# Optimization experiments

Hardware: AMD Instinct MI355X
Metric: run time of the kernel (lower is better)

Reference implementation:

```python
import jax, jax.numpy as jnp
import numpy as np

B, N, DIM = 8, 512, 768
H, DH = 12, 64
INNER = H * DH
MLP = 3072
DEPTH = 4
EPS = 1e-5
LS = 0.1  # LayerScale init_eps for depth <= 18


def _ln(x, scale):
    # flax LayerNorm(use_bias=False): (x-mean)/sqrt(var+eps) * scale
    mu = jnp.mean(x, axis=-1, keepdims=True)
    var = jnp.mean(jnp.square(x - mu), axis=-1, keepdims=True)
    return (x - mu) * jax.lax.rsqrt(var + EPS) * scale


def setup_inputs() -> dict:
    key = jax.random.key(0)
    ks = jax.random.split(key, 13)
    s = 0.02
    inp = {
        "x": jax.random.normal(ks[0], (B, N, DIM), jnp.float32),
        "ln1": jnp.ones((DEPTH, DIM), jnp.float32),
        "Wq": jax.random.normal(ks[1], (DEPTH, DIM, INNER), jnp.float32) * s,
        "Wkv": jax.random.normal(ks[2], (DEPTH, DIM, 2 * INNER), jnp.float32) * s,
        "mix_pre": jax.random.normal(ks[3], (DEPTH, H, H), jnp.float32) * 0.1,
        "mix_post": jax.random.normal(ks[4], (DEPTH, H, H), jnp.float32) * 0.1,
        "Wo": jax.random.normal(ks[5], (DEPTH, INNER, DIM), jnp.float32) * s,
        "bo": jnp.zeros((DEPTH, DIM), jnp.float32),
        "ln2": jnp.ones((DEPTH, DIM), jnp.float32),
        "W1": jax.random.normal(ks[6], (DEPTH, DIM, MLP), jnp.float32) * s,
        "b1": jnp.zeros((DEPTH, MLP), jnp.float32),
        "W2": jax.random.normal(ks[7], (DEPTH, MLP, DIM), jnp.float32) * s,
        "b2": jnp.zeros((DEPTH, DIM), jnp.float32),
    }
    return inp


def _block(x, p):
    ln1, Wq, Wkv, mp, mq, Wo, bo, ln2, W1, b1, W2, b2 = p
    scale = DH ** -0.5
    h = _ln(x, ln1)
    q = h @ Wq                                  # [b,n,inner]
    kv = h @ Wkv
    k, v = jnp.split(kv, 2, axis=-1)
    def to_heads(t):
        return t.reshape(B, N, H, DH).transpose(0, 2, 1, 3)  # b h n d
    q, k, v = to_heads(q), to_heads(k), to_heads(v)
    dots = jnp.einsum('bhid,bhjd->bhij', q, k) * scale
    dots = jnp.einsum('bhij,hg->bgij', dots, mp)   # talking-heads pre-softmax
    attn = jax.nn.softmax(dots, axis=-1)
    attn = jnp.einsum('bhij,hg->bgij', attn, mq)   # talking-heads post-softmax
    o = jnp.einsum('bhij,bhjd->bhid', attn, v)
    o = o.transpose(0, 2, 1, 3).reshape(B, N, INNER)
    x = (o @ Wo + bo) * LS + x
    h2 = _ln(x, ln2)
    x = ((jax.nn.gelu(h2 @ W1 + b1) @ W2) + b2) * LS + x
    return x, None


def reference(x, ln1, Wq, Wkv, mix_pre, mix_post, Wo, bo, ln2, W1, b1, W2, b2):
    params = (ln1, Wq, Wkv, mix_pre, mix_post, Wo, bo, ln2, W1, b1, W2, b2)
    out, _ = jax.lax.scan(_block, x, params)
    return out
```

## Files before the change

### kernel.cpp

```cpp
#include <hip/hip_runtime.h>


#define LSCALE 0.1f

typedef __bf16 bf16;
typedef __bf16 bf16x8 __attribute__((ext_vector_type(8)));
typedef __bf16 bf16x4 __attribute__((ext_vector_type(4)));
typedef unsigned short ushort4v __attribute__((ext_vector_type(4)));
typedef float  f32x4  __attribute__((ext_vector_type(4)));

__device__ __forceinline__ void g2l16(const void* g, void* l) {
    __builtin_amdgcn_global_load_lds(
        (const __attribute__((address_space(1))) void*)g,
        (__attribute__((address_space(3))) void*)l, 16, 0, 0);
}

__device__ __forceinline__ void tconv_tile(int T, int t,
    const float* __restrict__ Wq, const float* __restrict__ Wkv,
    const float* __restrict__ Wo, const float* __restrict__ W1,
    const float* __restrict__ W2, bf16* __restrict__ WtAll, char* pmem)
{
    float (*st)[65] = (float(*)[65])pmem;
    const int L = T / 1728;
    int bx = T - L * 1728;
    bf16* WtL = WtAll + (long)L * 7077888;
    const float* src; bf16* dst; int K, N, ntn;
    if (bx < 144) {
        src = Wq + (long)L * 589824;   dst = WtL;            K = 768;  N = 768;  ntn = 12;
    } else if (bx < 432) {
        bx -= 144;
        src = Wkv + (long)L * 1179648; dst = WtL + 589824;   K = 768;  N = 1536; ntn = 24;
    } else if (bx < 576) {
        bx -= 432;
        src = Wo + (long)L * 589824;   dst = WtL + 1769472;  K = 768;  N = 768;  ntn = 12;
    } else if (bx < 1152) {
        bx -= 576;
        src = W1 + (long)L * 2359296;  dst = WtL + 2359296;  K = 768;  N = 3072; ntn = 48;
    } else {
        bx -= 1152;
        src = W2 + (long)L * 2359296;  dst = WtL + 4718592;  K = 3072; N = 768;  ntn = 12;
    }
    const int n0 = (bx % ntn) * 64, k0 = (bx / ntn) * 64;
    const int r = t >> 4, c4 = (t & 15) * 4;
#pragma unroll
    for (int rr = 0; rr < 4; rr++) {
        const f32x4 v = *(const f32x4*)(src + (long)(k0 + r + rr * 16) * N + n0 + c4);
        st[r + rr * 16][c4 + 0] = v[0];
        st[r + rr * 16][c4 + 1] = v[1];
        st[r + rr * 16][c4 + 2] = v[2];
        st[r + rr * 16][c4 + 3] = v[3];
    }
    __syncthreads();
    const int kc = (t & 7) * 8;
#pragma unroll
    for (int p = 0; p < 2; p++) {
        const int n = p * 32 + (t >> 3);
        bf16x8 o;
#pragma unroll
        for (int e = 0; e < 8; e++) o[e] = (bf16)st[kc + e][n];
        *(bf16x8*)(dst + (long)(n0 + n) * K + k0 + kc) = o;
    }
}

template<int EPI, bool PLANA = false, bool RID = false>
__global__ __launch_bounds__(256, 2)
void gemm_bt(const bf16* __restrict__ A, int lda, long saz1, long saz2,
             const bf16* __restrict__ Bt, int ldb, long sbz1, long sbz2,
             void* __restrict__ Cv, int ldc, long scz1, long scz2,
             int M, int N, int K, int zmod,
             const float* __restrict__ bias, float scale,
             int mt, int nt, int rbase,
             const float* __restrict__ tWq, const float* __restrict__ tWkv,
             const float* __restrict__ tWo, const float* __restrict__ tW1,
             const float* __restrict__ tW2, bf16* __restrict__ tWt)
{
    __shared__ __align__(16) char smem[35840];
    bf16* As = (bf16*)smem;
    bf16* Bs = (bf16*)(smem + 16384);
    bf16* Cs = (bf16*)smem;

    int bm, bn, z;
    if constexpr (RID) {
        const int nbg = mt * nt * zmod;
        const int bx = blockIdx.x;
        if (bx >= nbg) {
            tconv_tile(rbase + bx - nbg, threadIdx.x,
                       tWq, tWkv, tWo, tW1, tW2, tWt, smem);
            return;
        }
        bm = bx % mt;
        const int r = bx / mt;
        bn = r % nt;
        z  = r / nt;
    } else {
        bm = blockIdx.x; bn = blockIdx.y; z = blockIdx.z;
    }

    const int z1 = z / zmod, z2 = z - z1 * zmod;
    const bf16* Ab = A  + saz1 * (long)z1 + saz2 * (long)z2;
    const bf16* Bb = Bt + sbz1 * (long)z1 + sbz2 * (long)z2;

    const int m0 = bm * 128, n0 = bn * 128;
    const int tid = threadIdx.x, w = tid >> 6, l = tid & 63;
    const int wr = (w >> 1) * 64, wc = (w & 1) * 64;
    const int lr = l & 15, lq = l >> 4;
    const int srow = l >> 2, scol8 = (l & 3) * 8;

    long abase = 0;
    if constexpr (PLANA)
        abase = (long)(m0 >> 9) * 393216 + (long)((m0 & 511) + w * 32) * 64;

    f32x4 acc[4][4];
#pragma unroll
    for (int i = 0; i < 4; i++)
#pragma unroll
        for (int j = 0; j < 4; j++)
#pragma unroll
            for (int r = 0; r < 4; r++) acc[i][j][r] = 0.f;

    for (int k0 = 0; k0 < K; k0 += 64) {
        const bf16* Ag;
        int ldaa;
        if constexpr (PLANA) {
            Ag = Ab + abase + ((long)(k0 >> 6)) * 32768;
            ldaa = 64;
        } else {
            Ag = Ab + (long)(m0 + w * 32) * lda + k0;
            ldaa = lda;
        }
        const bf16* Bg = Bb + (long)(n0 + w * 32) * ldb + k0;
        g2l16(Ag + (long)srow * ldaa + scol8,             As + w * 1024);
        g2l16(Ag + (long)(srow + 16) * ldaa + scol8,      As + w * 1024 + 512);
        g2l16(Ag + (long)srow * ldaa + 32 + scol8,        As + 4096 + w * 1024);
        g2l16(Ag + (long)(srow + 16) * ldaa + 32 + scol8, As + 4096 + w * 1024 + 512);
        g2l16(Bg + (long)srow * ldb + scol8,             Bs + w * 1024);
        g2l16(Bg + (long)(srow + 16) * ldb + scol8,      Bs + w * 1024 + 512);
        g2l16(Bg + (long)srow * ldb + 32 + scol8,        Bs + 4096 + w * 1024);
        g2l16(Bg + (long)(srow + 16) * ldb + 32 + scol8, Bs + 4096 + w * 1024 + 512);
        __syncthreads();

#pragma unroll
        for (int hh = 0; hh < 2; hh++) {
            bf16x8 fa[4], fb[4];
#pragma unroll
            for (int i = 0; i < 4; i++)
                fa[i] = *(const bf16x8*)(As + hh * 4096 + (wr + i * 16 + lr) * 32 + lq * 8);
#pragma unroll
            for (int i = 0; i < 4; i++)
                fb[i] = *(const bf16x8*)(Bs + hh * 4096 + (wc + i * 16 + lr) * 32 + lq * 8);
#pragma unroll
            for (int mi = 0; mi < 4; mi++)
#pragma unroll
                for (int ni = 0; ni < 4; ni++)
                    acc[mi][ni] = __builtin_amdgcn_mfma_f32_16x16x32_bf16(
                        fa[mi], fb[ni], acc[mi][ni], 0, 0, 0);
        }
        __syncthreads();
    }

#pragma unroll
    for (int ni = 0; ni < 4; ni++) {
        const int col = wc + ni * 16 + lr;
        float bv = 0.f;
        if (EPI == 1) bv = bias[n0 + col];
#pragma unroll
        for (int mi = 0; mi < 4; mi++) {
#pragma unroll
            for (int r = 0; r < 4; r++) {
                const int row = wr + mi * 16 + lq * 4 + r;
                float v = acc[mi][ni][r];
                if (EPI == 0) {
                    v *= scale;
                } else if (EPI == 1) {
                    const float xx = v + bv;
                    const float u  = 0.7978845608f * (xx + 0.044715f * xx * xx * xx);
                    const float th = 1.f - 2.f / (__expf(2.f * u) + 1.f);
                    v = 0.5f * xx * (1.f + th);
                }
                Cs[row * 136 + col] = (bf16)v;
            }
        }
    }
    __syncthreads();

    const long cb = scz1 * (long)z1 + scz2 * (long)z2;
    const int rrow = tid >> 4, cg = tid & 15;
#pragma unroll
    for (int p = 0; p < 8; p++) {
        const int row = p * 16 + rrow;
        const bf16x8 v = *(const bf16x8*)(Cs + row * 136 + cg * 8);
        *(bf16x8*)((bf16*)Cv + cb + (long)(m0 + row) * ldc + n0 + cg * 8) = v;
    }
}

template<int PLANO>
__global__ __launch_bounds__(256, 4)
void gemm_av(const bf16* __restrict__ S, const bf16* __restrict__ qkvc,
             bf16* __restrict__ oc)
{
    __shared__ __align__(16) char av_smem[9728];
    bf16* As  = (bf16*)av_smem;
    bf16* Bst = (bf16*)(av_smem + 4096);
    bf16* Cs  = (bf16*)av_smem;

    const int z = blockIdx.y, b = z / 12, g = z - b * 12;
    const bf16* Ab;
    int sld;
    if constexpr (PLANO) {
        Ab = S + (long)b * 3145728 + g * 512;
        sld = 6144;
    } else {
        Ab = S + (long)z * 262144;
        sld = 512;
    }
    const bf16* Bb = qkvc + (long)b * 1179648 + 1536 + g * 64;

    const int i0 = blockIdx.x * 64;
    const int tid = threadIdx.x, w = tid >> 6, l = tid & 63;
    const int lr = l & 15, lq = l >> 4;
    const int srow = l >> 2, scol8 = (l & 3) * 8;
    const int kp = tid >> 4, dq = tid & 15;
    const int kcol = ((((kp >> 2) ^ ((dq >> 1) & 3)) << 3) | ((kp & 3) << 1));

    f32x4 acc[4];
#pragma unroll
    for (int j = 0; j < 4; j++)
#pragma unroll
        for (int r = 0; r < 4; r++) acc[j][r] = 0.f;

    unsigned short* Bw = (unsigned short*)Bst;

    for (int k0 = 0; k0 < 512; k0 += 32) {
        const bf16* Ag = Ab + (long)(i0 + w * 16) * sld + k0;
        g2l16(Ag + (long)srow * sld + scol8, As + w * 512);

        const bf16* Bg = Bb + (long)(k0 + 2 * kp) * 2304 + dq * 4;
        ushort4v u0 = *(const ushort4v*)(Bg);
        ushort4v u1 = *(const ushort4v*)(Bg + 2304);
#pragma unroll
        for (int r = 0; r < 4; r++) {
            unsigned p = (unsigned)u0[r] | ((unsigned)u1[r] << 16);
            *(unsigned*)(Bw + (dq * 4 + r) * 40 + kcol) = p;
        }
        __syncthreads();

        bf16x8 fa = *(const bf16x8*)(As + (w * 16 + lr) * 32 + lq * 8);
        bf16x8 fb[4];
#pragma unroll
        for (int i = 0; i < 4; i++) {
            const int d = i * 16 + lr;
            fb[i] = *(const bf16x8*)(Bst + d * 40 + ((lq ^ ((d >> 3) & 3)) << 3));
        }
#pragma unroll
        for (int ni = 0; ni < 4; ni++)
            acc[ni] = __builtin_amdgcn_mfma_f32_16x16x32_bf16(
                fa, fb[ni], acc[ni], 0, 0, 0);
        __syncthreads();
    }

    if constexpr (PLANO) {
#pragma unroll
        for (int ni = 0; ni < 4; ni++)
#pragma unroll
            for (int r = 0; r < 4; r++)
                Cs[(w * 16 + lq * 4 + r) * 68 + ni * 16 + lr] = (bf16)acc[ni][r];
        __syncthreads();
        const int rr = tid >> 2, c16 = (tid & 3) * 16;
        bf16* orow = oc + ((long)z * 512 + i0 + rr) * 64 + c16;
        *(bf16x8*)(orow)     = *(const bf16x8*)(Cs + rr * 68 + c16);
        *(bf16x8*)(orow + 8) = *(const bf16x8*)(Cs + rr * 68 + c16 + 8);
    } else {
        bf16* Cb = oc + (long)b * 1179648 + g * 64;
#pragma unroll
        for (int ni = 0; ni < 4; ni++) {
            const int gc = ni * 16 + lr;
#pragma unroll
            for (int r = 0; r < 4; r++) {
                const int gr = i0 + w * 16 + lq * 4 + r;
                Cb[(long)gr * 2304 + gc] = (bf16)acc[ni][r];
            }
        }
    }
}

__global__ __launch_bounds__(256)
void tconv_k(const float* __restrict__ in, bf16* __restrict__ out,
             int K, int N)
{
    __shared__ float t[32][33];
    const int n0 = blockIdx.x * 32, k0 = blockIdx.y * 32;
    const int x = threadIdx.x, y = threadIdx.y;
#pragma unroll
    for (int yy = 0; yy < 4; yy++)
        t[y + yy * 8][x] = in[(long)(k0 + y + yy * 8) * N + n0 + x];
    __syncthreads();
#pragma unroll
    for (int yy = 0; yy < 4; yy++)
        out[(long)(n0 + y + yy * 8) * K + k0 + x] = (bf16)t[x][y + yy * 8];
}

__global__ __launch_bounds__(256)
void pre2_k(const float* __restrict__ Wq, const float* __restrict__ Wkv,
            const float* __restrict__ Wo, const float* __restrict__ W1,
            const float* __restrict__ W2, bf16* __restrict__ WtAll,
            const float* __restrict__ x, float* __restrict__ xf,
            const float* __restrict__ gam, bf16* __restrict__ hout)
{
    __shared__ __align__(16) char pmem[16640];
    const int bxg = blockIdx.x;
    const int t = threadIdx.x;
    if (bxg < 432) {
        tconv_tile(bxg, t, Wq, Wkv, Wo, W1, W2, WtAll, pmem);
    } else {
        const int row = bxg - 432;
        float* ps  = (float*)pmem;
        float* pss = (float*)pmem + 4;
        const float* xin = x + (long)row * 768;
        float* xr = xf + (long)row * 768;
        float v[3];
#pragma unroll
        for (int i = 0; i < 3; i++) {
            const int c = t + i * 256;
            const float xv = xin[c];
            xr[c] = xv;
            v[i] = xv;
        }
        float s  = v[0] + v[1] + v[2];
        float ss = v[0] * v[0] + v[1] * v[1] + v[2] * v[2];
#pragma unroll
        for (int off = 32; off; off >>= 1) {
            s  += __shfl_xor(s, off);
            ss += __shfl_xor(ss, off);
        }
        const int wv = t >> 6, l = t & 63;
        if (l == 0) { ps[wv] = s; pss[wv] = ss; }
        __syncthreads();
        s  = ps[0] + ps[1] + ps[2] + ps[3];
        ss = pss[0] + pss[1] + pss[2] + pss[3];
        const float mu = s * (1.f / 768.f);
        const float rs = rsqrtf(ss * (1.f / 768.f) - mu * mu + 1e-5f);
        bf16* orow = hout + (long)row * 768;
#pragma unroll
        for (int i = 0; i < 3; i++) {
            const int c = t + i * 256;
            orow[c] = (bf16)((v[i] - mu) * rs * gam[c]);
        }
    }
}

__global__ __launch_bounds__(256)
void lnres_k(float* __restrict__ xf, const bf16* __restrict__ P0,
             const bf16* __restrict__ P1, const float* __restrict__ bias,
             const float* __restrict__ gam, bf16* __restrict__ out,
             const float* __restrict__ src)
{
    const int row = blockIdx.x, t = threadIdx.x;
    float* xr = xf + (long)row * 768;
    float v[3];
#pragma unroll
    for (int i = 0; i < 3; i++) {
        const int c = t + i * 256;
        float xv;
        if (src) {
            xv = src[(long)row * 768 + c];
            xr[c] = xv;
        } else if (P0) {
            xv = xr[c] + LSCALE * ((float)P0[(long)row * 768 + c] +
                                   (float)P1[(long)row * 768 + c] + bias[c]);
            xr[c] = xv;
        } else {
            xv = xr[c];
        }
        v[i] = xv;
    }
    float s  = v[0] + v[1] + v[2];
    float ss = v[0] * v[0] + v[1] * v[1] + v[2] * v[2];
#pragma unroll
    for (int off = 32; off; off >>= 1) {
        s  += __shfl_xor(s, off);
        ss += __shfl_xor(ss, off);
    }
    __shared__ float ps[4], pss[4];
    const int wv = t >> 6, l = t & 63;
    if (l == 0) { ps[wv] = s; pss[wv] = ss; }
    __syncthreads();
    s  = ps[0] + ps[1] + ps[2] + ps[3];
    ss = pss[0] + pss[1] + pss[2] + pss[3];
    const float mu = s * (1.f / 768.f);
    const float rs = rsqrtf(ss * (1.f / 768.f) - mu * mu + 1e-5f);
    bf16* orow = out + (long)row * 768;
#pragma unroll
    for (int i = 0; i < 3; i++) {
        const int c = t + i * 256;
        orow[c] = (bf16)((v[i] - mu) * rs * gam[c]);
    }
}

__global__ __launch_bounds__(256)
void outres_k(const float* __restrict__ xf, const bf16* __restrict__ P0,
              const bf16* __restrict__ P1, const float* __restrict__ bias,
              float* __restrict__ out)
{
    const long i4 = ((long)blockIdx.x * 256 + threadIdx.x) * 4;
    const int c = (int)(i4 % 768);
    const f32x4 xv = *(const f32x4*)(xf + i4);
    const bf16x4 p0 = *(const bf16x4*)(P0 + i4);
    const bf16x4 p1 = *(const bf16x4*)(P1 + i4);
    const f32x4 bv = *(const f32x4*)(bias + c);
    f32x4 o;
#pragma unroll
    for (int e = 0; e < 4; e++)
        o[e] = xv[e] + LSCALE * ((float)p0[e] + (float)p1[e] + bv[e]);
    *(f32x4*)(out + i4) = o;
}

template<int CONTIG>
__global__ __launch_bounds__(256)
void mixsm_k(bf16* __restrict__ S, const float* __restrict__ mp,
             const float* __restrict__ mq)
{
    __shared__ float buf[12][512];
    __shared__ float rds[12];
    const int b = blockIdx.y, i = blockIdx.x, t = threadIdx.x;
    const long pstr = CONTIG ? 512 : 262144;
    bf16* Sb = CONTIG ? S + ((long)b * 512 + i) * 6144
                      : S + ((long)b * 12 * 512 + i) * 512;

    float s0[12], s1[12];
#pragma unroll
    for (int h = 0; h < 12; h++) {
        union { unsigned u; bf16 v[2]; } p;
        p.u = *(const unsigned*)(Sb + h * pstr + 2 * t);
        s0[h] = (float)p.v[0];
        s1[h] = (float)p.v[1];
    }
#pragma unroll
    for (int g = 0; g < 12; g++) {
        float a0 = 0.f, a1 = 0.f;
#pragma unroll
        for (int h = 0; h < 12; h++) {
            const float m = mp[h * 12 + g];
            a0 += s0[h] * m;
            a1 += s1[h] * m;
        }
        *(float2*)(&buf[g][2 * t]) = make_float2(a0, a1);
    }
    __syncthreads();

    const int wv = t >> 6, l = t & 63;
    for (int g = wv; g < 12; g += 4) {
        float mx = -3.0e38f;
#pragma unroll
        for (int k = 0; k < 8; k++) mx = fmaxf(mx, buf[g][l + 64 * k]);
#pragma unroll
        for (int off = 32; off; off >>= 1) mx = fmaxf(mx, __shfl_xor(mx, off));
        float sm = 0.f;
#pragma unroll
        for (int k = 0; k < 8; k++) {
            const float e = __expf(buf[g][l + 64 * k] - mx);
            buf[g][l + 64 * k] = e;
            sm += e;
        }
#pragma unroll
        for (int off = 32; off; off >>= 1) sm += __shfl_xor(sm, off);
        if (l == 0) rds[g] = 1.f / sm;
    }
    __syncthreads();

    float e0[12], e1[12];
#pragma unroll
    for (int h = 0; h < 12; h++) {
        const float2 ee = *(const float2*)(&buf[h][2 * t]);
        const float rd = rds[h];
        e0[h] = ee.x * rd;
        e1[h] = ee.y * rd;
    }
#pragma unroll
    for (int g = 0; g < 12; g++) {
        float a0 = 0.f, a1 = 0.f;
#pragma unroll
        for (int h = 0; h < 12; h++) {
            const float m = mq[h * 12 + g];
            a0 += e0[h] * m;
            a1 += e1[h] * m;
        }
        union { unsigned u; bf16 v[2]; } p;
        p.v[0] = (bf16)a0;
        p.v[1] = (bf16)a1;
        *(unsigned*)(Sb + g * pstr + 2 * t) = p.u;
    }
}

extern "C" void kernel_launch(void* const* d_in, const int* in_sizes, int n_in,
                              void* d_out, int out_size, void* d_ws, size_t ws_size,
                              hipStream_t stream)
{
    (void)in_sizes; (void)n_in; (void)out_size;
    const float* x   = (const float*)d_in[0];
    const float* ln1 = (const float*)d_in[1];
    const float* Wq  = (const float*)d_in[2];
    const float* Wkv = (const float*)d_in[3];
    const float* mp  = (const float*)d_in[4];
    const float* mq  = (const float*)d_in[5];
    const float* Wo  = (const float*)d_in[6];
    const float* bo  = (const float*)d_in[7];
    const float* ln2 = (const float*)d_in[8];
    const float* W1  = (const float*)d_in[9];
    const float* b1  = (const float*)d_in[10];
    const float* W2  = (const float*)d_in[11];
    const float* b2  = (const float*)d_in[12];

    char* ws = (char*)d_ws;
    float* xf  = (float*)(ws);
    bf16* h    = (bf16*)(ws + 12582912);
    bf16* qkv  = (bf16*)(ws + 18874368);
    bf16* S    = (bf16*)(ws + 37748736);
    bf16* mid  = S;
    bf16* P0   = h;
    bf16* P1w2 = qkv;
    bf16* P1wo = S;
    const long P1W2_OFF = 3145728;
    const long P1WO_OFF = 12582912;

    const dim3 tb(32, 8);

    if (ws_size >= 150994944ull) {
        bf16* WtAll = (bf16*)(ws + 88080384);
        bf16* oP    = (bf16*)(ws + 144703488);

        pre2_k<<<4528, 256, 0, stream>>>(Wq, Wkv, Wo, W1, W2, WtAll,
                                         x, xf, ln1, h);

        for (int L = 0; L < 4; L++) {
            bf16* WtL = WtAll + (long)L * 7077888;

            if (L > 0)
                lnres_k<<<4096, 256, 0, stream>>>(xf, P0, P1w2, b2 + (L - 1) * 768,
                                                  ln1 + L * 768, h, nullptr);

            if (L == 0)
                gemm_bt<0, false, true><<<576 + 1728, 256, 0, stream>>>(
                    h, 768, 0, 0, WtL, 768, 0, 0,
                    qkv, 2304, 0, 0, 4096, 2304, 768, 1, nullptr, 1.f,
                    32, 18, 432, Wq, Wkv, Wo, W1, W2, WtAll);
            else
                gemm_bt<0><<<dim3(32, 18, 1), 256, 0, stream>>>(
                    h, 768, 0, 0, WtL, 768, 0, 0,
                    qkv, 2304, 0, 0, 4096, 2304, 768, 1, nullptr, 1.f,
                    0, 0, 0, nullptr, nullptr, nullptr, nullptr, nullptr, nullptr);

            gemm_bt<0><<<dim3(4, 4, 96), 256, 0, stream>>>(
                qkv,       2304, 1179648, 64,
                qkv + 768, 2304, 1179648, 64,
                S,         6144, 3145728, 512,
                512, 512, 64, 12, nullptr, 0.125f,
                0, 0, 0, nullptr, nullptr, nullptr, nullptr, nullptr, nullptr);

            mixsm_k<1><<<dim3(512, 8), 256, 0, stream>>>(S, mp + L * 144, mq + L * 144);

            gemm_av<1><<<dim3(8, 96), 256, 0, stream>>>(S, qkv, oP);

            gemm_bt<4, true><<<dim3(32, 6, 2), 256, 0, stream>>>(
                oP, 64, 0, 196608, WtL + 1769472, 768, 0, 384,
                P0, 768, 0, P1WO_OFF, 4096, 768, 384, 2, nullptr, 1.f,
                0, 0, 0, nullptr, nullptr, nullptr, nullptr, nullptr, nullptr);

            lnres_k<<<4096, 256, 0, stream>>>(xf, P0, P1wo, bo + L * 768,
                                              ln2 + L * 768, h, nullptr);

            if (L == 0)
                gemm_bt<1, false, true><<<768 + 1728, 256, 0, stream>>>(
                    h, 768, 0, 0, WtL + 2359296, 768, 0, 0,
                    mid, 3072, 0, 0, 4096, 3072, 768, 1, b1 + L * 3072, 1.f,
                    32, 24, 2160, Wq, Wkv, Wo, W1, W2, WtAll);
            else if (L == 1)
                gemm_bt<1, false, true><<<768 + 1296, 256, 0, stream>>>(
                    h, 768, 0, 0, WtL + 2359296, 768, 0, 0,
                    mid, 3072, 0, 0, 4096, 3072, 768, 1, b1 + L * 3072, 1.f,
                    32, 24, 5616, Wq, Wkv, Wo, W1, W2, WtAll);
            else
                gemm_bt<1><<<dim3(32, 24, 1), 256, 0, stream>>>(
                    h, 768, 0, 0, WtL + 2359296, 768, 0, 0,
                    mid, 3072, 0, 0, 4096, 3072, 768, 1, b1 + L * 3072, 1.f,
                    0, 0, 0, nullptr, nullptr, nullptr, nullptr, nullptr, nullptr);

            if (L == 0)
                gemm_bt<4, false, true><<<384 + 1728, 256, 0, stream>>>(
                    mid, 3072, 0, 1536, WtL + 4718592, 3072, 0, 1536,
                    P0, 768, 0, P1W2_OFF, 4096, 768, 1536, 2, nullptr, 1.f,
                    32, 6, 3888, Wq, Wkv, Wo, W1, W2, WtAll);
            else
                gemm_bt<4><<<dim3(32, 6, 2), 256, 0, stream>>>(
                    mid, 3072, 0, 1536, WtL + 4718592, 3072, 0, 1536,
                    P0, 768, 0, P1W2_OFF, 4096, 768, 1536, 2, nullptr, 1.f,
                    0, 0, 0, nullptr, nullptr, nullptr, nullptr, nullptr, nullptr);
        }
    } else {
        bf16* Wt = (bf16*)(ws + 62914560);

        for (int L = 0; L < 4; L++) {
            tconv_k<<<dim3(24, 24), tb, 0, stream>>>(Wq + (long)L * 589824, Wt, 768, 768);
            tconv_k<<<dim3(48, 24), tb, 0, stream>>>(Wkv + (long)L * 1179648, Wt + 589824, 768, 1536);

            if (L == 0)
                lnres_k<<<4096, 256, 0, stream>>>(xf, nullptr, nullptr, nullptr,
                                                  ln1 + L * 768, h, x);
            else
                lnres_k<<<4096, 256, 0, stream>>>(xf, P0, P1w2, b2 + (L - 1) * 768,
                                                  ln1 + L * 768, h, nullptr);

            gemm_bt<0><<<dim3(32, 18, 1), 256, 0, stream>>>(
                h, 768, 0, 0, Wt, 768, 0, 0,
                qkv, 2304, 0, 0, 4096, 2304, 768, 1, nullptr, 1.f,
                0, 0, 0, nullptr, nullptr, nullptr, nullptr, nullptr, nullptr);

            for (int c = 0; c < 2; c++) {
                const long qb = (long)c * 4718592;
                gemm_bt<0><<<dim3(4, 4, 48), 256, 0, stream>>>(
                    qkv + qb,       2304, 1179648, 64,
                    qkv + 768 + qb, 2304, 1179648, 64,
                    S,               512, 3145728, 262144,
                    512, 512, 64, 12, nullptr, 0.125f,
                    0, 0, 0, nullptr, nullptr, nullptr, nullptr, nullptr, nullptr);

                mixsm_k<0><<<dim3(512, 4), 256, 0, stream>>>(S, mp + L * 144, mq + L * 144);

                gemm_av<0><<<dim3(8, 48), 256, 0, stream>>>(S, qkv + qb, qkv + qb);
            }

            tconv_k<<<dim3(24, 24), tb, 0, stream>>>(Wo + (long)L * 589824, Wt, 768, 768);
            gemm_bt<4><<<dim3(32, 6, 2), 256, 0, stream>>>(
                qkv, 2304, 0, 384, Wt, 768, 0, 384,
                P0, 768, 0, P1WO_OFF, 4096, 768, 384, 2, nullptr, 1.f,
                0, 0, 0, nullptr, nullptr, nullptr, nullptr, nullptr, nullptr);

            lnres_k<<<4096, 256, 0, stream>>>(xf, P0, P1wo, bo + L * 768,
                                              ln2 + L * 768, h, nullptr);

            tconv_k<<<dim3(96, 24), tb, 0, stream>>>(W1 + (long)L * 2359296, Wt, 768, 3072);
            gemm_bt<1><<<dim3(32, 24, 1), 256, 0, stream>>>(
                h, 768, 0, 0, Wt, 768, 0, 0,
                mid, 3072, 0, 0, 4096, 3072, 768, 1, b1 + L * 3072, 1.f,
                0, 0, 0, nullptr, nullptr, nullptr, nullptr, nullptr, nullptr);

            tconv_k<<<dim3(24, 96), tb, 0, stream>>>(W2 + (long)L * 2359296, Wt, 3072, 768);
            gemm_bt<4><<<dim3(32, 6, 2), 256, 0, stream>>>(
                mid, 3072, 0, 1536, Wt, 3072, 0, 1536,
                P0, 768, 0, P1W2_OFF, 4096, 768, 1536, 2, nullptr, 1.f,
                0, 0, 0, nullptr, nullptr, nullptr, nullptr, nullptr, nullptr);
        }
    }

    outres_k<<<3072, 256, 0, stream>>>(xf, P0, P1w2, b2 + 3 * 768, (float*)d_out);
}
```

Baseline: 858.6 us.

## Add XCD-aware block remapping and direct-register path for K=64 QK^T GEMM

```diff
diff --git a/kernel.cpp b/kernel.cpp
--- a/kernel.cpp
+++ b/kernel.cpp
@@ -62,7 +62,7 @@
     }
 }
 
-template<int EPI, bool PLANA = false, bool RID = false>
+template<int EPI, bool PLANA = false, bool RID = false, bool DIR = false>
 __global__ __launch_bounds__(256, 2)
 void gemm_bt(const bf16* __restrict__ A, int lda, long saz1, long saz2,
              const bf16* __restrict__ Bt, int ldb, long sbz1, long sbz2,
@@ -80,6 +80,7 @@
     bf16* Cs = (bf16*)smem;
 
     int bm, bn, z;
+    int bid, mt_, nt_, zt_;
     if constexpr (RID) {
         const int nbg = mt * nt * zmod;
         const int bx = blockIdx.x;
@@ -88,12 +89,28 @@
                        tWq, tWkv, tWo, tW1, tW2, tWt, smem);
             return;
         }
-        bm = bx % mt;
-        const int r = bx / mt;
-        bn = r % nt;
-        z  = r / nt;
-    } else {
-        bm = blockIdx.x; bn = blockIdx.y; z = blockIdx.z;
+        bid = bx; mt_ = mt; nt_ = nt; zt_ = zmod;
+    } else {
+        mt_ = gridDim.x; nt_ = gridDim.y; zt_ = gridDim.z;
+        bid = blockIdx.x + mt_ * (blockIdx.y + nt_ * (int)blockIdx.z);
+    }
+    if (!DIR && (mt_ & 7) == 0) {
+        const int nb = mt_ * nt_ * zt_;
+        const int q = nb >> 3, r = nb & 7;
+        const int xcd = bid & 7, i = bid >> 3;
+        const int u = (xcd < r) ? xcd * (q + 1) + i
+                                : r * (q + 1) + (xcd - r) * q + i;
+        const int csz = 8 * nt_ * zt_;
+        const int mc = u / csz, rem = u - mc * csz;
+        const int sub = rem >> 3;
+        bm = mc * 8 + (rem & 7);
+        bn = sub % nt_;
+        z  = sub / nt_;
+    } else {
+        bm = bid % mt_;
+        const int r2 = bid / mt_;
+        bn = r2 % nt_;
+        z  = r2 / nt_;
     }
 
     const int z1 = z / zmod, z2 = z - z1 * zmod;
@@ -118,6 +135,26 @@
 #pragma unroll
             for (int r = 0; r < 4; r++) acc[i][j][r] = 0.f;
 
+    if constexpr (DIR) {
+        const bf16* Agd = Ab + (long)m0 * lda;
+        const bf16* Bgd = Bb + (long)n0 * ldb;
+        bf16x8 fa[2][4], fb[2][4];
+#pragma unroll
+        for (int hh = 0; hh < 2; hh++)
+#pragma unroll
+            for (int i = 0; i < 4; i++) {
+                fa[hh][i] = *(const bf16x8*)(Agd + (long)(wr + i * 16 + lr) * lda + hh * 32 + lq * 8);
+                fb[hh][i] = *(const bf16x8*)(Bgd + (long)(wc + i * 16 + lr) * ldb + hh * 32 + lq * 8);
+            }
+#pragma unroll
+        for (int hh = 0; hh < 2; hh++)
+#pragma unroll
+            for (int mi = 0; mi < 4; mi++)
+#pragma unroll
+                for (int ni = 0; ni < 4; ni++)
+                    acc[mi][ni] = __builtin_amdgcn_mfma_f32_16x16x32_bf16(
+                        fa[hh][mi], fb[hh][ni], acc[mi][ni], 0, 0, 0);
+    } else {
     for (int k0 = 0; k0 < K; k0 += 64) {
         const bf16* Ag;
         int ldaa;
@@ -156,6 +193,7 @@
                         fa[mi], fb[ni], acc[mi][ni], 0, 0, 0);
         }
         __syncthreads();
+    }
     }
 
 #pragma unroll
@@ -549,7 +587,7 @@
                     qkv, 2304, 0, 0, 4096, 2304, 768, 1, nullptr, 1.f,
                     0, 0, 0, nullptr, nullptr, nullptr, nullptr, nullptr, nullptr);
 
-            gemm_bt<0><<<dim3(4, 4, 96), 256, 0, stream>>>(
+            gemm_bt<0, false, false, true><<<dim3(4, 4, 96), 256, 0, stream>>>(
                 qkv,       2304, 1179648, 64,
                 qkv + 768, 2304, 1179648, 64,
                 S,         6144, 3145728, 512,
```

Result: no change. 874.5 us (+1.9%).
